# Performance work log

Measured on AMD Instinct MI355X. Metric: run time of the kernel, lower is better.

Reference implementation:

```python
import jax, jax.numpy as jnp
import numpy as np

EMBEDDING_DIM = 64
N_EMBEDDINGS = 512


def setup_inputs() -> dict:
    key = jax.random.key(0)
    k1, k2 = jax.random.split(key)
    inputs = jax.random.normal(k1, (32, 64, 64, 64), dtype=jnp.float32)  # NCHW, C==embedding_dim
    weight = jax.random.normal(k2, (N_EMBEDDINGS, EMBEDDING_DIM), dtype=jnp.float32)
    return {"inputs": inputs, "weight": weight}


def reference(inputs, weight):
    # NCHW -> NHWC, flatten to [N, D]
    x = jnp.transpose(inputs, (0, 2, 3, 1))  # [B, H, W, D]
    in_shape = x.shape
    flat = x.reshape(-1, EMBEDDING_DIM)  # [N, D]

    distances = (
        jnp.sum(flat * flat, axis=1, keepdims=True)
        + jnp.sum(weight * weight, axis=1)
        - 2.0 * flat @ weight.T
    )
    idx = jnp.argmin(distances, axis=1)  # [N]

    # one-hot @ weight is just a gather
    quantized = weight[idx].reshape(in_shape)  # [B, H, W, D]

    # commitment loss: mse(stop_grad(quantized), x)
    e_latent_loss = jnp.mean(jnp.square(jax.lax.stop_gradient(quantized) - x))

    # straight-through estimator
    quantized = x + jax.lax.stop_gradient(quantized - x)

    return jnp.transpose(quantized, (0, 3, 1, 2)), e_latent_loss
```

## Files before the change

### kernel.cpp

```cpp
#include <hip/hip_runtime.h>
#include <math.h>

typedef short bf16x8 __attribute__((ext_vector_type(8)));
typedef float f32x4 __attribute__((ext_vector_type(4)));

#define VQ_D 64
#define VQ_K 512
#define VQ_NQ 131072
#define VQ_TOTAL 8388608
#define NT 32
#define TAU 8e-3f

__device__ __forceinline__ ushort bf16_rne(float f) {
    uint u = __builtin_bit_cast(uint, f);
    u += 0x7fffu + ((u >> 16) & 1u);
    return (ushort)(u >> 16);
}
__device__ __forceinline__ float bf16_to_f(ushort h) {
    uint u = ((uint)h) << 16;
    return __builtin_bit_cast(float, u);
}

__global__ __launch_bounds__(128) void vq_prep(const float* __restrict__ w,
                                               ushort* __restrict__ wfrag,
                                               float* __restrict__ wn,
                                               float* __restrict__ out) {
    if (blockIdx.x == 0 && threadIdx.x == 0) out[VQ_TOTAL] = 0.f;
    const int k = blockIdx.x * 128 + threadIdx.x;
    const float4* row = (const float4*)(w + k * VQ_D);
    const int t = k >> 4, col = k & 15;
    float nrm = 0.f;
    for (int g = 0; g < 8; ++g) {
        float4 a = row[2 * g], b4 = row[2 * g + 1];
        float v[8] = {a.x, a.y, a.z, a.w, b4.x, b4.y, b4.z, b4.w};
        ushort hi[8], lo[8];
#pragma unroll
        for (int j = 0; j < 8; ++j) {
            nrm = fmaf(v[j], v[j], nrm);
            hi[j] = bf16_rne(v[j]);
            lo[j] = bf16_rne(v[j] - bf16_to_f(hi[j]));
        }
        const int quad = g & 3, fh = g >> 2;
        const int lane = quad * 16 + col;
        bf16x8* basez = (bf16x8*)wfrag + t * 256 + lane;
        *(basez + fh * 64)       = *(bf16x8*)hi;
        *(basez + (2 + fh) * 64) = *(bf16x8*)lo;
    }
    wn[k] = nrm;
}

__global__ __launch_bounds__(256, 3) void vq_main(const float* __restrict__ in,
                                                  const float* __restrict__ w,
                                                  const ushort* __restrict__ wfrag,
                                                  const float* __restrict__ wng,
                                                  float* __restrict__ out) {
    __shared__ float xn_lds[128];
    __shared__ float best_lds[128], sec_lds[128];
    __shared__ int   bi_lds[128], si_lds[128];

    const int tid  = threadIdx.x;
    const int lane = tid & 63;
    const int wid  = tid >> 6;
    const int col  = lane & 15;
    const int quad = lane >> 4;
    const int n0  = blockIdx.x * 128;
    const int b   = n0 >> 12;
    const int hw0 = n0 & 4095;
    const float* xg0 = in + (b << 18) + hw0;
    const float* xgW = xg0 + wid * 32;

    bf16x8 ah0[2], ah1[2], al0[2], al1[2];
#pragma unroll
    for (int T = 0; T < 2; ++T) {
        const float* xq = xgW + T * 16 + col;
        float sx = 0.f;
        ushort h0[8], l0[8], h1[8], l1[8];
#pragma unroll
        for (int j = 0; j < 8; ++j) {
            float v0 = xq[(quad * 8 + j) << 12];
            float v1 = xq[(32 + quad * 8 + j) << 12];
            sx = fmaf(v0, v0, sx);
            sx = fmaf(v1, v1, sx);
            h0[j] = bf16_rne(v0); l0[j] = bf16_rne(v0 - bf16_to_f(h0[j]));
            h1[j] = bf16_rne(v1); l1[j] = bf16_rne(v1 - bf16_to_f(h1[j]));
        }
        ah0[T] = *(bf16x8*)h0; al0[T] = *(bf16x8*)l0;
        ah1[T] = *(bf16x8*)h1; al1[T] = *(bf16x8*)l1;
        sx += __shfl_xor(sx, 16, 64);
        sx += __shfl_xor(sx, 32, 64);
        if (quad == 0) xn_lds[wid * 32 + T * 16 + col] = sx;
    }

    float best[8], sec[8];
#pragma unroll
    for (int r = 0; r < 8; ++r) { best[r] = 3.0e38f; sec[r] = 3.0e38f; }

    const bf16x8* wf = (const bf16x8*)wfrag + lane;
    bf16x8 bh0 = wf[0], bh1 = wf[64], bl0 = wf[128], bl1 = wf[192];
    float wnv = wng[col];

#pragma unroll 1
    for (int t = 0; t < NT; ++t) {
        bf16x8 nh0, nh1, nl0, nl1;
        float wnn;
        if (t + 1 < NT) {
            const bf16x8* nx = wf + (t + 1) * 256;
            nh0 = nx[0]; nh1 = nx[64]; nl0 = nx[128]; nl1 = nx[192];
            wnn = wng[(t + 1) * 16 + col];
        }
#pragma unroll
        for (int T = 0; T < 2; ++T) {
            f32x4 accP = {0.f, 0.f, 0.f, 0.f}, accQ = {0.f, 0.f, 0.f, 0.f};
            accP = __builtin_amdgcn_mfma_f32_16x16x32_bf16(ah0[T], bh0, accP, 0, 0, 0);
            accP = __builtin_amdgcn_mfma_f32_16x16x32_bf16(ah1[T], bh1, accP, 0, 0, 0);
            accQ = __builtin_amdgcn_mfma_f32_16x16x32_bf16(ah0[T], bl0, accQ, 0, 0, 0);
            accQ = __builtin_amdgcn_mfma_f32_16x16x32_bf16(ah1[T], bl1, accQ, 0, 0, 0);
            accQ = __builtin_amdgcn_mfma_f32_16x16x32_bf16(al0[T], bh0, accQ, 0, 0, 0);
            accQ = __builtin_amdgcn_mfma_f32_16x16x32_bf16(al1[T], bh1, accQ, 0, 0, 0);
#pragma unroll
            for (int j = 0; j < 4; ++j) {
                float dist = fmaf(-2.f, accP[j] + accQ[j], wnv);
                uint u = (__builtin_bit_cast(uint, dist) & 0xFFFFFFE0u) | (uint)t;
                float key = __builtin_bit_cast(float, u);
                const int r = T * 4 + j;
                float m = fmaxf(best[r], key);
                best[r] = fminf(best[r], key);
                sec[r]  = fminf(sec[r], m);
            }
        }
        bh0 = nh0; bh1 = nh1; bl0 = nl0; bl1 = nl1; wnv = wnn;
    }

    float bD[8], sD[8];
    int bI[8], sI[8];
#pragma unroll
    for (int r = 0; r < 8; ++r) {
        uint ub = __builtin_bit_cast(uint, best[r]);
        uint us = __builtin_bit_cast(uint, sec[r]);
        bI[r] = (int)(ub & 31u) * 16 + col;
        sI[r] = (int)(us & 31u) * 16 + col;
        bD[r] = __builtin_bit_cast(float, ub & 0xFFFFFFE0u);
        sD[r] = __builtin_bit_cast(float, us & 0xFFFFFFE0u);
    }

#pragma unroll
    for (int off = 1; off < 16; off <<= 1) {
#pragma unroll
        for (int r = 0; r < 8; ++r) {
            float ob = __shfl_xor(bD[r], off, 64);
            float os = __shfl_xor(sD[r], off, 64);
            int   oi = __shfl_xor(bI[r], off, 64);
            int   oc = __shfl_xor(sI[r], off, 64);
            bool oWins = (ob < bD[r]) || (ob == bD[r] && oi < bI[r]);
            float nb  = oWins ? ob    : bD[r];
            int   ni  = oWins ? oi    : bI[r];
            float c1  = oWins ? bD[r] : ob;
            int   ci1 = oWins ? bI[r] : oi;
            float c2  = oWins ? os    : sD[r];
            int   ci2 = oWins ? oc    : sI[r];
            bool c1w = (c1 < c2) || (c1 == c2 && ci1 < ci2);
            sD[r] = c1w ? c1  : c2;
            sI[r] = c1w ? ci1 : ci2;
            bD[r] = nb; bI[r] = ni;
        }
    }
    if (col == 0) {
#pragma unroll
        for (int r = 0; r < 8; ++r) {
            const int q = wid * 32 + (r >> 2) * 16 + quad * 4 + (r & 3);
            best_lds[q] = bD[r]; sec_lds[q] = sD[r];
            bi_lds[q] = bI[r];   si_lds[q] = sI[r];
        }
    }
    __syncthreads();

    if (tid < 128) {
        const int q = tid;
        float cb = best_lds[q], cs = sec_lds[q];
        int cbi = bi_lds[q], csi = si_lds[q];
        double chosen = (double)cb;
        if (cs - cb < TAU) {
            const float* wb  = w + cbi * VQ_D;
            const float* ws2 = w + csi * VQ_D;
            const float* xqp = xg0 + q;
            double nb = 0.0, dotb = 0.0, ns = 0.0, dots = 0.0;
            for (int d = 0; d < VQ_D; ++d) {
                double xv = (double)xqp[d << 12];
                double wbv = (double)wb[d], wsv = (double)ws2[d];
                nb = fma(wbv, wbv, nb); dotb = fma(xv, wbv, dotb);
                ns = fma(wsv, wsv, ns); dots = fma(xv, wsv, dots);
            }
            double db = nb - 2.0 * dotb, ds = ns - 2.0 * dots;
            if (ds < db || (ds == db && csi < cbi)) { cbi = csi; chosen = ds; }
            else                                    { chosen = db; }
        }
        bi_lds[q] = cbi;
        double lq = (double)xn_lds[q] + chosen;
#pragma unroll
        for (int off = 32; off > 0; off >>= 1)
            lq += __shfl_down(lq, off, 64);
        if ((tid & 63) == 0)
            atomicAdd(out + VQ_TOTAL, (float)(lq * (1.0 / (double)VQ_TOTAL)));
    }
    __syncthreads();

    {
        const int q = tid & 127, half = tid >> 7;
        const float4* wrow = (const float4*)(w + bi_lds[q] * VQ_D) + half * 8;
        float* op = out + (b << 18) + hw0 + q;
#pragma unroll
        for (int u = 0; u < 8; ++u) {
            float4 v = wrow[u];
            const int d = half * 32 + 4 * u;
            op[(d + 0) << 12] = v.x;
            op[(d + 1) << 12] = v.y;
            op[(d + 2) << 12] = v.z;
            op[(d + 3) << 12] = v.w;
        }
    }
}

extern "C" void kernel_launch(void* const* d_in, const int* in_sizes, int n_in,
                              void* d_out, int out_size, void* d_ws, size_t ws_size,
                              hipStream_t stream) {
    const float* in = (const float*)d_in[0];
    const float* w  = (const float*)d_in[1];
    float* out = (float*)d_out;

    ushort* wfrag = (ushort*)d_ws;
    float*  wn    = (float*)((char*)d_ws + 131072);

    vq_prep<<<4, 128, 0, stream>>>(w, wfrag, wn, out);
    vq_main<<<VQ_NQ / 128, 256, 0, stream>>>(in, w, wfrag, wn, out);
}
```

Baseline: 140.3 us.

## Stage codebook fragments through double-buffered LDS via global_load_lds

```diff
diff --git a/kernel.cpp b/kernel.cpp
--- a/kernel.cpp
+++ b/kernel.cpp
@@ -9,7 +9,18 @@
 #define VQ_NQ 131072
 #define VQ_TOTAL 8388608
 #define NT 32
+#define NC 16
 #define TAU 8e-3f
+
+typedef __attribute__((address_space(1))) void as1_void;
+typedef __attribute__((address_space(3))) void as3_void;
+
+__device__ __forceinline__ void gll16(const void* g, void* l) {
+    __builtin_amdgcn_global_load_lds((as1_void*)(void*)g, (as3_void*)l, 16, 0, 0);
+}
+__device__ __forceinline__ void gll4(const void* g, void* l) {
+    __builtin_amdgcn_global_load_lds((as1_void*)(void*)g, (as3_void*)l, 4, 0, 0);
+}
 
 __device__ __forceinline__ ushort bf16_rne(float f) {
     uint u = __builtin_bit_cast(uint, f);
@@ -26,34 +37,38 @@
                                                float* __restrict__ wn,
                                                float* __restrict__ out) {
     if (blockIdx.x == 0 && threadIdx.x == 0) out[VQ_TOTAL] = 0.f;
-    const int k = blockIdx.x * 128 + threadIdx.x;
+    const int tid = threadIdx.x;
+    const int k = (blockIdx.x << 4) + (tid >> 3);
+    const int g = tid & 7;
     const float4* row = (const float4*)(w + k * VQ_D);
+    float4 a = row[2 * g], b4 = row[2 * g + 1];
+    float v[8] = {a.x, a.y, a.z, a.w, b4.x, b4.y, b4.z, b4.w};
+    ushort hi[8], lo[8];
+    float nrm = 0.f;
+#pragma unroll
+    for (int j = 0; j < 8; ++j) {
+        nrm = fmaf(v[j], v[j], nrm);
+        hi[j] = bf16_rne(v[j]);
+        lo[j] = bf16_rne(v[j] - bf16_to_f(hi[j]));
+    }
+    nrm += __shfl_xor(nrm, 1, 64);
+    nrm += __shfl_xor(nrm, 2, 64);
+    nrm += __shfl_xor(nrm, 4, 64);
+    if (g == 0) wn[k] = nrm;
     const int t = k >> 4, col = k & 15;
-    float nrm = 0.f;
-    for (int g = 0; g < 8; ++g) {
-        float4 a = row[2 * g], b4 = row[2 * g + 1];
-        float v[8] = {a.x, a.y, a.z, a.w, b4.x, b4.y, b4.z, b4.w};
-        ushort hi[8], lo[8];
-#pragma unroll
-        for (int j = 0; j < 8; ++j) {
-            nrm = fmaf(v[j], v[j], nrm);
-            hi[j] = bf16_rne(v[j]);
-            lo[j] = bf16_rne(v[j] - bf16_to_f(hi[j]));
-        }
-        const int quad = g & 3, fh = g >> 2;
-        const int lane = quad * 16 + col;
-        bf16x8* basez = (bf16x8*)wfrag + t * 256 + lane;
-        *(basez + fh * 64)       = *(bf16x8*)hi;
-        *(basez + (2 + fh) * 64) = *(bf16x8*)lo;
-    }
-    wn[k] = nrm;
-}
-
-__global__ __launch_bounds__(256, 3) void vq_main(const float* __restrict__ in,
+    const int quad = g & 3, fh = g >> 2;
+    bf16x8* basez = (bf16x8*)wfrag + t * 256 + quad * 16 + col;
+    basez[fh * 64]       = *(bf16x8*)hi;
+    basez[(2 + fh) * 64] = *(bf16x8*)lo;
+}
+
+__global__ __launch_bounds__(256, 4) void vq_main(const float* __restrict__ in,
                                                   const float* __restrict__ w,
                                                   const ushort* __restrict__ wfrag,
                                                   const float* __restrict__ wng,
                                                   float* __restrict__ out) {
+    __shared__ __align__(16) char bstage[2][8192];
+    __shared__ float wn_lds[VQ_K];
     __shared__ float xn_lds[128];
     __shared__ float best_lds[128], sec_lds[128];
     __shared__ int   bi_lds[128], si_lds[128];
@@ -69,6 +84,15 @@
     const float* xg0 = in + (b << 18) + hw0;
     const float* xgW = xg0 + wid * 32;
 
+    {
+        const char* gs = (const char*)wfrag + tid * 16;
+        char* lb = &bstage[0][0] + wid * 1024;
+        gll16(gs, lb);
+        gll16(gs + 4096, lb + 4096);
+        gll4(wng + tid,       (char*)wn_lds + wid * 256);
+        gll4(wng + 256 + tid, (char*)wn_lds + 1024 + wid * 256);
+    }
+
     bf16x8 ah0[2], ah1[2], al0[2], al1[2];
 #pragma unroll
     for (int T = 0; T < 2; ++T) {
@@ -91,44 +115,54 @@
         if (quad == 0) xn_lds[wid * 32 + T * 16 + col] = sx;
     }
 
+    __syncthreads();
+
     float best[8], sec[8];
 #pragma unroll
     for (int r = 0; r < 8; ++r) { best[r] = 3.0e38f; sec[r] = 3.0e38f; }
 
-    const bf16x8* wf = (const bf16x8*)wfrag + lane;
-    bf16x8 bh0 = wf[0], bh1 = wf[64], bl0 = wf[128], bl1 = wf[192];
-    float wnv = wng[col];
-
 #pragma unroll 1
-    for (int t = 0; t < NT; ++t) {
-        bf16x8 nh0, nh1, nl0, nl1;
-        float wnn;
-        if (t + 1 < NT) {
-            const bf16x8* nx = wf + (t + 1) * 256;
-            nh0 = nx[0]; nh1 = nx[64]; nl0 = nx[128]; nl1 = nx[192];
-            wnn = wng[(t + 1) * 16 + col];
-        }
-#pragma unroll
-        for (int T = 0; T < 2; ++T) {
-            f32x4 accP = {0.f, 0.f, 0.f, 0.f}, accQ = {0.f, 0.f, 0.f, 0.f};
-            accP = __builtin_amdgcn_mfma_f32_16x16x32_bf16(ah0[T], bh0, accP, 0, 0, 0);
-            accP = __builtin_amdgcn_mfma_f32_16x16x32_bf16(ah1[T], bh1, accP, 0, 0, 0);
-            accQ = __builtin_amdgcn_mfma_f32_16x16x32_bf16(ah0[T], bl0, accQ, 0, 0, 0);
-            accQ = __builtin_amdgcn_mfma_f32_16x16x32_bf16(ah1[T], bl1, accQ, 0, 0, 0);
-            accQ = __builtin_amdgcn_mfma_f32_16x16x32_bf16(al0[T], bh0, accQ, 0, 0, 0);
-            accQ = __builtin_amdgcn_mfma_f32_16x16x32_bf16(al1[T], bh1, accQ, 0, 0, 0);
-#pragma unroll
-            for (int j = 0; j < 4; ++j) {
-                float dist = fmaf(-2.f, accP[j] + accQ[j], wnv);
-                uint u = (__builtin_bit_cast(uint, dist) & 0xFFFFFFE0u) | (uint)t;
-                float key = __builtin_bit_cast(float, u);
-                const int r = T * 4 + j;
-                float m = fmaxf(best[r], key);
-                best[r] = fminf(best[r], key);
-                sec[r]  = fminf(sec[r], m);
+    for (int t = 0; t < NC; ++t) {
+        char* const bcur = &bstage[t & 1][0];
+        if (t + 1 < NC) {
+            const char* gs = (const char*)wfrag + (t + 1) * 8192 + tid * 16;
+            char* lb = &bstage[(t + 1) & 1][0] + wid * 1024;
+            gll16(gs, lb);
+            gll16(gs + 4096, lb + 4096);
+        }
+#pragma unroll
+        for (int s = 0; s < 2; ++s) {
+            const int t2 = 2 * t + s;
+            const char* rb = bcur + s * 4096 + lane * 16;
+            bf16x8 bh0 = *(const bf16x8*)(rb);
+            bf16x8 bh1 = *(const bf16x8*)(rb + 1024);
+            bf16x8 bl0 = *(const bf16x8*)(rb + 2048);
+            bf16x8 bl1 = *(const bf16x8*)(rb + 3072);
+            const float wnv = wn_lds[t2 * 16 + col];
+#pragma unroll
+            for (int T = 0; T < 2; ++T) {
+                f32x4 accP = {0.f, 0.f, 0.f, 0.f}, accQ = {0.f, 0.f, 0.f, 0.f};
+                __builtin_amdgcn_s_setprio(1);
+                accP = __builtin_amdgcn_mfma_f32_16x16x32_bf16(ah0[T], bh0, accP, 0, 0, 0);
+                accP = __builtin_amdgcn_mfma_f32_16x16x32_bf16(ah1[T], bh1, accP, 0, 0, 0);
+                accQ = __builtin_amdgcn_mfma_f32_16x16x32_bf16(ah0[T], bl0, accQ, 0, 0, 0);
+                accQ = __builtin_amdgcn_mfma_f32_16x16x32_bf16(ah1[T], bl1, accQ, 0, 0, 0);
+                accQ = __builtin_amdgcn_mfma_f32_16x16x32_bf16(al0[T], bh0, accQ, 0, 0, 0);
+                accQ = __builtin_amdgcn_mfma_f32_16x16x32_bf16(al1[T], bh1, accQ, 0, 0, 0);
+                __builtin_amdgcn_s_setprio(0);
+#pragma unroll
+                for (int j = 0; j < 4; ++j) {
+                    float dist = fmaf(-2.f, accP[j] + accQ[j], wnv);
+                    uint u = (__builtin_bit_cast(uint, dist) & 0xFFFFFFE0u) | (uint)t2;
+                    float key = __builtin_bit_cast(float, u);
+                    const int r = T * 4 + j;
+                    float m = fmaxf(best[r], key);
+                    best[r] = fminf(best[r], key);
+                    sec[r]  = fminf(sec[r], m);
+                }
             }
         }
-        bh0 = nh0; bh1 = nh1; bl0 = nl0; bl1 = nl1; wnv = wnn;
+        __syncthreads();
     }
 
     float bD[8], sD[8];
@@ -230,6 +264,6 @@
     ushort* wfrag = (ushort*)d_ws;
     float*  wn    = (float*)((char*)d_ws + 131072);
 
-    vq_prep<<<4, 128, 0, stream>>>(w, wfrag, wn, out);
+    vq_prep<<<32, 128, 0, stream>>>(w, wfrag, wn, out);
     vq_main<<<VQ_NQ / 128, 256, 0, stream>>>(in, w, wfrag, wn, out);
 }
```

Measured after the change: 132.6 us. 1.06x faster.
